# Performance work log

Measured on AMD Instinct MI355X. Metric: run time of the kernel, lower is better.

Reference implementation:

```python
import jax, jax.numpy as jnp
import numpy as np

D_MODEL = 1024
N_HEADS = 16
HEAD_DIM = D_MODEL // N_HEADS
B, T = 4, 2048


def setup_inputs() -> dict:
    key = jax.random.key(0)
    ks = jax.random.split(key, 5)
    s = 1.0 / np.sqrt(D_MODEL)
    return {
        "x": jax.random.normal(ks[0], (B, T, D_MODEL), dtype=jnp.float32),
        "Wq": jax.random.normal(ks[1], (D_MODEL, D_MODEL), dtype=jnp.float32) * s,
        "bq": jnp.zeros((D_MODEL,), jnp.float32),
        "Wk": jax.random.normal(ks[2], (D_MODEL, D_MODEL), dtype=jnp.float32) * s,
        "bk": jnp.zeros((D_MODEL,), jnp.float32),
        "Wv": jax.random.normal(ks[3], (D_MODEL, D_MODEL), dtype=jnp.float32) * s,
        "bv": jnp.zeros((D_MODEL,), jnp.float32),
        "Wo": jax.random.normal(ks[4], (D_MODEL, D_MODEL), dtype=jnp.float32) * s,
        "bo": jnp.zeros((D_MODEL,), jnp.float32),
    }


def reference(x, Wq, bq, Wk, bk, Wv, bv, Wo, bo):
    Bx, Tx, C = x.shape
    H, Dh = N_HEADS, HEAD_DIM
    # projections (torch Linear: y = x @ W.T + b)
    q = (x @ Wq.T + bq).reshape(Bx, Tx, H, Dh).transpose(0, 2, 1, 3)  # [B,H,T,Dh]
    k = (x @ Wk.T + bk).reshape(Bx, Tx, H, Dh).transpose(0, 2, 1, 3)
    v = (x @ Wv.T + bv).reshape(Bx, Tx, H, Dh).transpose(0, 2, 1, 3)
    scores = jnp.einsum("bhqd,bhkd->bhqk", q, k) / np.sqrt(Dh).astype(np.float32)
    causal = jnp.tril(jnp.ones((Tx, Tx), dtype=bool))
    scores = jnp.where(causal, scores, -jnp.inf)
    attn = jax.nn.softmax(scores, axis=-1)  # dropout in eval mode = identity
    y = jnp.einsum("bhqk,bhkd->bhqd", attn, v)
    y = y.transpose(0, 2, 1, 3).reshape(Bx, Tx, C)
    return y @ Wo.T + bo
```

## Files before the change

kernel.cpp:

```cpp
#include <hip/hip_runtime.h>

typedef __attribute__((ext_vector_type(8))) short short8;
typedef __attribute__((ext_vector_type(4))) float f32x4;
typedef unsigned short u16;
typedef unsigned int u32;

#define NH 16

#if __has_builtin(__builtin_amdgcn_exp2f)
#define EXP2(x) __builtin_amdgcn_exp2f(x)
#else
#define EXP2(x) exp2f(x)
#endif

__device__ __forceinline__ u32 f2bf(float f) {
  u32 u = __builtin_bit_cast(u32, f);
  return (u + 0x7fffu + ((u >> 16) & 1u)) >> 16;
}

__device__ __forceinline__ u32 cvtpk(float lo, float hi) {
  u32 r;
  asm("v_cvt_pk_bf16_f32 %0, %1, %2" : "=v"(r) : "v"(lo), "v"(hi));
  return r;
}

__device__ __forceinline__ void gload_lds16(const u16* g, u16* l) {
  __builtin_amdgcn_global_load_lds(
      (const __attribute__((address_space(1))) void*)g,
      (__attribute__((address_space(3))) void*)l, 16, 0, 0);
}

__global__ __launch_bounds__(256) void k_convert(
    const float* __restrict__ x, const float* __restrict__ wq,
    const float* __restrict__ wk, const float* __restrict__ wv,
    const float* __restrict__ wo, u16* __restrict__ dst) {
  int i = blockIdx.x * 256 + threadIdx.x;
  size_t e = (size_t)i * 4;
  const float* s; size_t off;
  if (e < 8388608ull)       { s = x;  off = e; }
  else if (e < 9437184ull)  { s = wq; off = e - 8388608ull; }
  else if (e < 10485760ull) { s = wk; off = e - 9437184ull; }
  else if (e < 11534336ull) { s = wv; off = e - 10485760ull; }
  else                      { s = wo; off = e - 11534336ull; }
  float4 d = *(const float4*)(s + off);
  uint2 o;
  o.x = cvtpk(d.x, d.y);
  o.y = cvtpk(d.z, d.w);
  *(uint2*)(dst + e) = o;
}

#define GPHASE(MH, NH_, LA, LB)                                                \
  if (LA) {                                                                    \
    _Pragma("unroll")                                                          \
    for (int mt = 0; mt < 4; ++mt)                                             \
      _Pragma("unroll")                                                        \
      for (int ks = 0; ks < 2; ++ks)                                           \
        af[mt][ks] = *(const short8*)(Ab +                                     \
            (wr * MT * 16 + ((MH) * 4 + mt) * 16 + l16) * 64 +                 \
            ((ks * 4 + quad) ^ swz) * 8);                                      \
  }                                                                            \
  if (LB) {                                                                    \
    _Pragma("unroll")                                                          \
    for (int nt = 0; nt < NH2; ++nt)                                           \
      _Pragma("unroll")                                                        \
      for (int ks = 0; ks < 2; ++ks)                                           \
        bfr[nt][ks] = *(const short8*)(Bb +                                    \
            (wn * NT * 16 + ((NH_) * NH2 + nt) * 16 + l16) * 64 +              \
            ((ks * 4 + quad) ^ swz) * 8);                                      \
  }                                                                            \
  __builtin_amdgcn_s_barrier();                                                \
  __builtin_amdgcn_s_setprio(1);                                               \
  _Pragma("unroll")                                                            \
  for (int mt = 0; mt < 4; ++mt)                                               \
    _Pragma("unroll")                                                          \
    for (int nt = 0; nt < NH2; ++nt)                                           \
      _Pragma("unroll")                                                        \
      for (int ks = 0; ks < 2; ++ks)                                           \
        acc[(MH) * 4 + mt][(NH_) * NH2 + nt] =                                 \
            __builtin_amdgcn_mfma_f32_16x16x32_bf16(                           \
                af[mt][ks], bfr[nt][ks], acc[(MH) * 4 + mt][(NH_) * NH2 + nt], \
                0, 0, 0);                                                      \
  __builtin_amdgcn_s_setprio(0);                                               \
  __builtin_amdgcn_s_barrier();                                                \
  __builtin_amdgcn_sched_barrier(0);

#define STAGE_T(T, PB)                                                         \
  {                                                                            \
    const u16* aT = aTh + (T) * 64;                                            \
    const u16* bT = bTh + (T) * 64;                                            \
    u16* aD = &As[PB][0] + dbase;                                              \
    u16* bD = &Bs[PB][0] + dbase;                                              \
    _Pragma("unroll")                                                          \
    for (int j = 0; j < NLA; ++j) gload_lds16(aT + j * 65536, aD + j * 4096);  \
    _Pragma("unroll")                                                          \
    for (int j = 0; j < NLB; ++j) gload_lds16(bT + j * 65536, bD + j * 4096);  \
  }

template <int MT, int NT>
__device__ __forceinline__ void gemm_core(const u16* __restrict__ Aptr,
                                          const u16* __restrict__ Bptr,
                                          int m0, int n0,
                                          f32x4 (&acc)[MT][NT]) {
  constexpr int NLA = MT / 2;
  constexpr int NLB = NT;
  constexpr int NLD = NLA + NLB;
  constexpr int NH2 = NT / 2;
  __shared__ u16 As[2][MT * 32 * 64];
  __shared__ u16 Bs[2][NT * 64 * 64];
  const int tid = threadIdx.x;
  const int wave = tid >> 6, lane = tid & 63;
  const int quad = lane >> 4, l16 = lane & 15;
  const int wr = wave >> 2, wn = wave & 3;
  const int swz = l16 & 7;
  const int srow = tid >> 3;
  const int srcg = (tid & 7) ^ (srow & 7);
  const u16* aTh = Aptr + (size_t)(m0 + srow) * 1024 + srcg * 8;
  const u16* bTh = Bptr + (size_t)(n0 + srow) * 1024 + srcg * 8;
  const int dbase = wave * 512;

  {
    f32x4 z = {0.f, 0.f, 0.f, 0.f};
    #pragma unroll
    for (int a = 0; a < MT; ++a)
      #pragma unroll
      for (int b2 = 0; b2 < NT; ++b2) acc[a][b2] = z;
  }

  STAGE_T(0, 0)

  short8 af[4][2], bfr[NH2][2];
  for (int t = 0; t < 16; ++t) {
    const int p = t & 1;
    if (t < 15) {
      STAGE_T(t + 1, p ^ 1)
      if constexpr (NLD == 8)
        asm volatile("s_waitcnt vmcnt(8)" ::: "memory");
      else if constexpr (NLD == 6)
        asm volatile("s_waitcnt vmcnt(6)" ::: "memory");
      else if constexpr (NLD == 4)
        asm volatile("s_waitcnt vmcnt(4)" ::: "memory");
      else
        asm volatile("s_waitcnt vmcnt(0)" ::: "memory");
    } else {
      asm volatile("s_waitcnt vmcnt(0)" ::: "memory");
    }
    __builtin_amdgcn_s_barrier();
    __builtin_amdgcn_sched_barrier(0);
    const u16* Ab = &As[p][0];
    const u16* Bb = &Bs[p][0];
    if constexpr (MT == 8) {
      GPHASE(0, 0, true, true)
      GPHASE(0, 1, false, true)
      GPHASE(1, 1, true, false)
      GPHASE(1, 0, false, true)
    } else {
      GPHASE(0, 0, true, true)
      GPHASE(0, 1, false, true)
    }
  }
}

__global__ __launch_bounds__(512, 2) void k_gemm_qkv(
    const u16* __restrict__ A, const u16* __restrict__ W,
    const float* __restrict__ bq, const float* __restrict__ bk,
    const float* __restrict__ bv, u16* __restrict__ qkv,
    u16* __restrict__ vt) {
  const int bid = blockIdx.x;
  const int xw = (bid & 7) * 96 + (bid >> 3);
  const int mtile = xw / 12, ntile = xw % 12;
  const int m0 = mtile * 128, n0 = ntile * 256;
  const int z = n0 >> 10;
  const float* bias = (z == 0) ? bq : (z == 1) ? bk : bv;
  u16* out = qkv + (size_t)z * 8388608;
  const float scl = (z == 0) ? 0.125f * 1.44269504088896340736f : 1.0f;
  f32x4 acc[4][4];
  gemm_core<4, 4>(A, W, m0, n0, acc);
  const int tid = threadIdx.x;
  const int wave = tid >> 6, lane = tid & 63;
  const int quad = lane >> 4, l16 = lane & 15;
  const int wr = wave >> 2, wn = wave & 3;
  if (z == 2) {
    #pragma unroll
    for (int mt = 0; mt < 4; ++mt) {
      #pragma unroll
      for (int nt = 0; nt < 4; ++nt) {
        int nn = (n0 + wn * 64 + nt * 16 + l16) & 1023;
        float bn = bias[nn];
        int h = nn >> 6, d = nn & 63;
        int mbase = m0 + wr * 64 + mt * 16 + quad * 4;
        int b = mbase >> 11, tb = mbase & 2047;
        uint2 pk;
        pk.x = cvtpk(acc[mt][nt][0] + bn, acc[mt][nt][1] + bn);
        pk.y = cvtpk(acc[mt][nt][2] + bn, acc[mt][nt][3] + bn);
        *(uint2*)(vt + ((size_t)(b * NH + h) * 64 + d) * 2048 + tb) = pk;
      }
    }
  } else {
    #pragma unroll
    for (int mt = 0; mt < 4; ++mt) {
      #pragma unroll
      for (int nt = 0; nt < 4; ++nt) {
        int nn = (n0 + wn * 64 + nt * 16 + l16) & 1023;
        float bn = bias[nn];
        int h = nn >> 6, d = nn & 63;
        #pragma unroll
        for (int r = 0; r < 4; ++r) {
          int m = m0 + wr * 64 + mt * 16 + quad * 4 + r;
          int b = m >> 11, tt = m & 2047;
          float val = (acc[mt][nt][r] + bn) * scl;
          out[(((size_t)(b * NH + h) * 2048 + tt) << 6) + d] = (u16)f2bf(val);
        }
      }
    }
  }
}

__global__ __launch_bounds__(512, 2) void k_gemm_out(
    const u16* __restrict__ A, const u16* __restrict__ Bw,
    const float* __restrict__ bias, float* __restrict__ out) {
  const int bid = blockIdx.x;
  const int sw = (bid & 7) * 32 + (bid >> 3);
  const int mtile = sw >> 3, ntile = sw & 7;
  const int m0 = mtile * 256, n0 = ntile * 128;
  f32x4 acc[8][2];
  gemm_core<8, 2>(A, Bw, m0, n0, acc);
  const int tid = threadIdx.x;
  const int wave = tid >> 6, lane = tid & 63;
  const int quad = lane >> 4, l16 = lane & 15;
  const int wr = wave >> 2, wn = wave & 3;
  #pragma unroll
  for (int mt = 0; mt < 8; ++mt) {
    #pragma unroll
    for (int nt = 0; nt < 2; ++nt) {
      int n = n0 + wn * 32 + nt * 16 + l16;
      float bn = bias[n];
      #pragma unroll
      for (int r = 0; r < 4; ++r) {
        int m = m0 + wr * 128 + mt * 16 + quad * 4 + r;
        out[(size_t)m * 1024 + n] = acc[mt][nt][r] + bn;
      }
    }
  }
}

#define ATTN_SUB(P, QF0, QF1, O, MI, LI, DIAG)                                 \
  {                                                                            \
    f32x4 st[4];                                                               \
    _Pragma("unroll")                                                          \
    for (int nt = 0; nt < 4; ++nt) {                                           \
      short8 kf0 = *(const short8*)(&Ks[P][(nt * 16 + l16) * 72 + quad * 8]);  \
      short8 kf1 = *(const short8*)(&Ks[P][(nt * 16 + l16) * 72 + 32 + quad * 8]); \
      f32x4 z4 = {0.f, 0.f, 0.f, 0.f};                                         \
      z4 = __builtin_amdgcn_mfma_f32_16x16x32_bf16(kf0, QF0, z4, 0, 0, 0);     \
      st[nt] = __builtin_amdgcn_mfma_f32_16x16x32_bf16(kf1, QF1, z4, 0, 0, 0); \
    }                                                                          \
    if (DIAG) {                                                                \
      int q_loc = wave * 16 + l16;                                             \
      _Pragma("unroll")                                                        \
      for (int nt = 0; nt < 4; ++nt) {                                         \
        _Pragma("unroll")                                                      \
        for (int r = 0; r < 4; ++r) {                                          \
          int k_loc = nt * 16 + quad * 4 + r;                                  \
          if (k_loc > q_loc) st[nt][r] = -1e30f;                               \
        }                                                                      \
      }                                                                        \
    }                                                                          \
    float mq[4];                                                               \
    _Pragma("unroll")                                                          \
    for (int nt = 0; nt < 4; ++nt)                                             \
      mq[nt] = fmaxf(fmaxf(st[nt][0], st[nt][1]), fmaxf(st[nt][2], st[nt][3]));\
    float mx = fmaxf(fmaxf(mq[0], mq[1]), fmaxf(mq[2], mq[3]));                \
    mx = fmaxf(mx, __shfl_xor(mx, 16, 64));                                    \
    mx = fmaxf(mx, __shfl_xor(mx, 32, 64));                                    \
    float mnew = fmaxf(MI, mx);                                                \
    float alpha = EXP2(MI - mnew);                                             \
    MI = mnew;                                                                 \
    LI *= alpha;                                                               \
    _Pragma("unroll")                                                          \
    for (int r = 0; r < 4; ++r) {                                              \
      float av = __shfl(alpha, quad * 4 + r, 16);                              \
      _Pragma("unroll")                                                        \
      for (int dt = 0; dt < 4; ++dt) O[dt][r] *= av;                           \
    }                                                                          \
    u32 Wx[4], Wy[4];                                                          \
    float sq[4];                                                               \
    _Pragma("unroll")                                                          \
    for (int nt = 0; nt < 4; ++nt) {                                           \
      float p0 = EXP2(st[nt][0] - mnew);                                       \
      float p1 = EXP2(st[nt][1] - mnew);                                       \
      float p2 = EXP2(st[nt][2] - mnew);                                       \
      float p3 = EXP2(st[nt][3] - mnew);                                       \
      sq[nt] = (p0 + p1) + (p2 + p3);                                          \
      Wx[nt] = cvtpk(p0, p1);                                                  \
      Wy[nt] = cvtpk(p2, p3);                                                  \
    }                                                                          \
    float sum = (sq[0] + sq[1]) + (sq[2] + sq[3]);                             \
    sum += __shfl_xor(sum, 16, 64);                                            \
    sum += __shfl_xor(sum, 32, 64);                                            \
    LI += sum;                                                                 \
    uint4 t0, t1;                                                              \
    {                                                                          \
      u32 e, f;                                                                \
      e = __shfl(Wx[0], s0, 64); f = __shfl(Wx[1], s0, 64); t0.x = hi ? f : e; \
      e = __shfl(Wy[0], s0, 64); f = __shfl(Wy[1], s0, 64); t0.y = hi ? f : e; \
      e = __shfl(Wx[0], s1, 64); f = __shfl(Wx[1], s1, 64); t0.z = hi ? f : e; \
      e = __shfl(Wy[0], s1, 64); f = __shfl(Wy[1], s1, 64); t0.w = hi ? f : e; \
      e = __shfl(Wx[2], s0, 64); f = __shfl(Wx[3], s0, 64); t1.x = hi ? f : e; \
      e = __shfl(Wy[2], s0, 64); f = __shfl(Wy[3], s0, 64); t1.y = hi ? f : e; \
      e = __shfl(Wx[2], s1, 64); f = __shfl(Wx[3], s1, 64); t1.z = hi ? f : e; \
      e = __shfl(Wy[2], s1, 64); f = __shfl(Wy[3], s1, 64); t1.w = hi ? f : e; \
    }                                                                          \
    short8 pf0 = __builtin_bit_cast(short8, t0);                               \
    short8 pf1 = __builtin_bit_cast(short8, t1);                               \
    _Pragma("unroll")                                                          \
    for (int dt = 0; dt < 4; ++dt) {                                           \
      short8 vf0 = *(const short8*)(&Vs[P][(dt * 16 + l16) * 72 + quad * 8]);  \
      short8 vf1 = *(const short8*)(&Vs[P][(dt * 16 + l16) * 72 + 32 + quad * 8]); \
      O[dt] = __builtin_amdgcn_mfma_f32_16x16x32_bf16(pf0, vf0, O[dt], 0, 0, 0); \
      O[dt] = __builtin_amdgcn_mfma_f32_16x16x32_bf16(pf1, vf1, O[dt], 0, 0, 0); \
    }                                                                          \
  }

#define ATTN_EPI(O, LI, QT)                                                    \
  _Pragma("unroll")                                                            \
  for (int r = 0; r < 4; ++r) {                                                \
    float lv = __shfl(LI, quad * 4 + r, 16);                                   \
    float inv = 1.0f / lv;                                                     \
    int t = (QT) * 64 + wave * 16 + quad * 4 + r;                              \
    _Pragma("unroll")                                                          \
    for (int dt = 0; dt < 4; ++dt) {                                           \
      int d = dt * 16 + l16;                                                   \
      y[(((size_t)b * 2048 + t) * NH + h) * 64 + d] = (u16)f2bf(O[dt][r] * inv); \
    }                                                                          \
  }

__global__ __launch_bounds__(256, 4) void k_attn(
    const u16* __restrict__ q, const u16* __restrict__ k,
    const u16* __restrict__ vt, u16* __restrict__ y) {
  const int tid = threadIdx.x;
  const int wave = tid >> 6, lane = tid & 63;
  const int quad = lane >> 4, l16 = lane & 15;
  const int bh = blockIdx.x, bx = blockIdx.y;
  const int qtB = bx, qtA = 31 - bx;
  const int b = bh >> 4, h = bh & 15;

  __shared__ u16 Ks[2][64 * 72];
  __shared__ u16 Vs[2][64 * 72];

  const u16* qbA = q + ((size_t)bh * 2048 + qtA * 64 + wave * 16 + l16) * 64;
  short8 qA0 = *(const short8*)(qbA + quad * 8);
  short8 qA1 = *(const short8*)(qbA + 32 + quad * 8);
  const u16* qbB = q + ((size_t)bh * 2048 + qtB * 64 + wave * 16 + l16) * 64;
  short8 qB0 = *(const short8*)(qbB + quad * 8);
  short8 qB1 = *(const short8*)(qbB + 32 + quad * 8);

  f32x4 oA[4], oB[4];
  {
    f32x4 z = {0.f, 0.f, 0.f, 0.f};
    #pragma unroll
    for (int dt = 0; dt < 4; ++dt) { oA[dt] = z; oB[dt] = z; }
  }
  float mA = -1e30f, lA = 0.f, mB = -1e30f, lB = 0.f;

  const u16* kbase = k + (size_t)bh * 131072;
  const u16* vbase = vt + (size_t)bh * 131072;
  const int r0 = tid >> 3, cc = tid & 7;
  const int s0 = ((quad & 1) << 5) + l16, s1 = s0 + 16;
  const int hi = quad >> 1;

  {
    uint4 k0 = *(const uint4*)(kbase + (size_t)r0 * 64 + cc * 8);
    uint4 k1 = *(const uint4*)(kbase + (size_t)(r0 + 32) * 64 + cc * 8);
    uint4 v0 = *(const uint4*)(vbase + (size_t)r0 * 2048 + cc * 8);
    uint4 v1 = *(const uint4*)(vbase + (size_t)(r0 + 32) * 2048 + cc * 8);
    *(uint4*)(&Ks[0][r0 * 72 + cc * 8]) = k0;
    *(uint4*)(&Ks[0][(r0 + 32) * 72 + cc * 8]) = k1;
    *(uint4*)(&Vs[0][r0 * 72 + cc * 8]) = v0;
    *(uint4*)(&Vs[0][(r0 + 32) * 72 + cc * 8]) = v1;
  }
  __syncthreads();

  for (int kt = 0; kt <= qtA; ++kt) {
    const int p = kt & 1;
    const bool pre = (kt < qtA);
    uint4 kr0, kr1, vr0, vr1;
    if (pre) {
      const u16* kb = kbase + (size_t)(kt + 1) * 4096;
      const u16* vb = vbase + (kt + 1) * 64;
      kr0 = *(const uint4*)(kb + (size_t)r0 * 64 + cc * 8);
      kr1 = *(const uint4*)(kb + (size_t)(r0 + 32) * 64 + cc * 8);
      vr0 = *(const uint4*)(vb + (size_t)r0 * 2048 + cc * 8);
      vr1 = *(const uint4*)(vb + (size_t)(r0 + 32) * 2048 + cc * 8);
    }

    ATTN_SUB(p, qA0, qA1, oA, mA, lA, (kt == qtA))
    if (kt <= qtB) {
      ATTN_SUB(p, qB0, qB1, oB, mB, lB, (kt == qtB))
    }

    if (pre) {
      *(uint4*)(&Ks[p ^ 1][r0 * 72 + cc * 8]) = kr0;
      *(uint4*)(&Ks[p ^ 1][(r0 + 32) * 72 + cc * 8]) = kr1;
      *(uint4*)(&Vs[p ^ 1][r0 * 72 + cc * 8]) = vr0;
      *(uint4*)(&Vs[p ^ 1][(r0 + 32) * 72 + cc * 8]) = vr1;
    }
    __syncthreads();
  }

  ATTN_EPI(oA, lA, qtA)
  ATTN_EPI(oB, lB, qtB)
}

extern "C" void kernel_launch(void* const* d_in, const int* in_sizes, int n_in,
                              void* d_out, int out_size, void* d_ws, size_t ws_size,
                              hipStream_t stream) {
  const float* x  = (const float*)d_in[0];
  const float* Wq = (const float*)d_in[1];
  const float* bq = (const float*)d_in[2];
  const float* Wk = (const float*)d_in[3];
  const float* bk = (const float*)d_in[4];
  const float* Wv = (const float*)d_in[5];
  const float* bv = (const float*)d_in[6];
  const float* Wo = (const float*)d_in[7];
  const float* bo = (const float*)d_in[8];
  float* out = (float*)d_out;

  u16* ws  = (u16*)d_ws;
  u16* xb  = ws;
  u16* Wb  = ws + 8388608;
  u16* qkv = ws + 12582912;
  u16* vt  = ws + 37748736;
  u16* y   = ws + 46137344;

  k_convert<<<dim3(12288), dim3(256), 0, stream>>>(x, Wq, Wk, Wv, Wo, ws);
  k_gemm_qkv<<<dim3(768), dim3(512), 0, stream>>>(xb, Wb, bq, bk, bv, qkv, vt);
  k_attn<<<dim3(64, 16), dim3(256), 0, stream>>>(qkv, qkv + 8388608, vt, y);
  k_gemm_out<<<dim3(256), dim3(512), 0, stream>>>(y, Wb + 3 * 1048576, bo, out);
}
```

Baseline: 297.5 us.

## Load K/V fragments directly from global memory and retile output GEMM

The attention kernel drops the LDS double-buffered K/V staging and its per-iteration barriers. Each wave now loads its MFMA K and V fragments straight from global memory into registers, relying on L1/L2 reuse across the four waves. The loop is also split into QK, softmax and PV stages so the two query tiles can interleave. Separately, the output projection GEMM changes its tile from 256x128 to 128x256. This trades LDS traffic and sync for more global/cache load instructions and higher register pressure.

```diff
diff --git a/kernel.cpp b/kernel.cpp
--- a/kernel.cpp
+++ b/kernel.cpp
@@ -220,39 +220,36 @@
     const float* __restrict__ bias, float* __restrict__ out) {
   const int bid = blockIdx.x;
   const int sw = (bid & 7) * 32 + (bid >> 3);
-  const int mtile = sw >> 3, ntile = sw & 7;
-  const int m0 = mtile * 256, n0 = ntile * 128;
-  f32x4 acc[8][2];
-  gemm_core<8, 2>(A, Bw, m0, n0, acc);
+  const int mtile = sw >> 2, ntile = sw & 3;
+  const int m0 = mtile * 128, n0 = ntile * 256;
+  f32x4 acc[4][4];
+  gemm_core<4, 4>(A, Bw, m0, n0, acc);
   const int tid = threadIdx.x;
   const int wave = tid >> 6, lane = tid & 63;
   const int quad = lane >> 4, l16 = lane & 15;
   const int wr = wave >> 2, wn = wave & 3;
   #pragma unroll
-  for (int mt = 0; mt < 8; ++mt) {
-    #pragma unroll
-    for (int nt = 0; nt < 2; ++nt) {
-      int n = n0 + wn * 32 + nt * 16 + l16;
+  for (int mt = 0; mt < 4; ++mt) {
+    #pragma unroll
+    for (int nt = 0; nt < 4; ++nt) {
+      int n = n0 + wn * 64 + nt * 16 + l16;
       float bn = bias[n];
       #pragma unroll
       for (int r = 0; r < 4; ++r) {
-        int m = m0 + wr * 128 + mt * 16 + quad * 4 + r;
+        int m = m0 + wr * 64 + mt * 16 + quad * 4 + r;
         out[(size_t)m * 1024 + n] = acc[mt][nt][r] + bn;
       }
     }
   }
 }
 
-#define ATTN_SUB(P, QF0, QF1, O, MI, LI, DIAG)                                 \
+#define QK_STEP(KF, QF0, QF1, ST, DIAG)                                        \
   {                                                                            \
-    f32x4 st[4];                                                               \
     _Pragma("unroll")                                                          \
     for (int nt = 0; nt < 4; ++nt) {                                           \
-      short8 kf0 = *(const short8*)(&Ks[P][(nt * 16 + l16) * 72 + quad * 8]);  \
-      short8 kf1 = *(const short8*)(&Ks[P][(nt * 16 + l16) * 72 + 32 + quad * 8]); \
       f32x4 z4 = {0.f, 0.f, 0.f, 0.f};                                         \
-      z4 = __builtin_amdgcn_mfma_f32_16x16x32_bf16(kf0, QF0, z4, 0, 0, 0);     \
-      st[nt] = __builtin_amdgcn_mfma_f32_16x16x32_bf16(kf1, QF1, z4, 0, 0, 0); \
+      z4 = __builtin_amdgcn_mfma_f32_16x16x32_bf16(KF[nt][0], QF0, z4, 0, 0, 0); \
+      ST[nt] = __builtin_amdgcn_mfma_f32_16x16x32_bf16(KF[nt][1], QF1, z4, 0, 0, 0); \
     }                                                                          \
     if (DIAG) {                                                                \
       int q_loc = wave * 16 + l16;                                             \
@@ -261,14 +258,18 @@
         _Pragma("unroll")                                                      \
         for (int r = 0; r < 4; ++r) {                                          \
           int k_loc = nt * 16 + quad * 4 + r;                                  \
-          if (k_loc > q_loc) st[nt][r] = -1e30f;                               \
+          if (k_loc > q_loc) ST[nt][r] = -1e30f;                               \
         }                                                                      \
       }                                                                        \
     }                                                                          \
+  }
+
+#define SM_STEP(ST, MI, LI, O, PF0, PF1)                                       \
+  {                                                                            \
     float mq[4];                                                               \
     _Pragma("unroll")                                                          \
     for (int nt = 0; nt < 4; ++nt)                                             \
-      mq[nt] = fmaxf(fmaxf(st[nt][0], st[nt][1]), fmaxf(st[nt][2], st[nt][3]));\
+      mq[nt] = fmaxf(fmaxf(ST[nt][0], ST[nt][1]), fmaxf(ST[nt][2], ST[nt][3]));\
     float mx = fmaxf(fmaxf(mq[0], mq[1]), fmaxf(mq[2], mq[3]));                \
     mx = fmaxf(mx, __shfl_xor(mx, 16, 64));                                    \
     mx = fmaxf(mx, __shfl_xor(mx, 32, 64));                                    \
@@ -286,10 +287,10 @@
     float sq[4];                                                               \
     _Pragma("unroll")                                                          \
     for (int nt = 0; nt < 4; ++nt) {                                           \
-      float p0 = EXP2(st[nt][0] - mnew);                                       \
-      float p1 = EXP2(st[nt][1] - mnew);                                       \
-      float p2 = EXP2(st[nt][2] - mnew);                                       \
-      float p3 = EXP2(st[nt][3] - mnew);                                       \
+      float p0 = EXP2(ST[nt][0] - mnew);                                       \
+      float p1 = EXP2(ST[nt][1] - mnew);                                       \
+      float p2 = EXP2(ST[nt][2] - mnew);                                       \
+      float p3 = EXP2(ST[nt][3] - mnew);                                       \
       sq[nt] = (p0 + p1) + (p2 + p3);                                          \
       Wx[nt] = cvtpk(p0, p1);                                                  \
       Wy[nt] = cvtpk(p2, p3);                                                  \
@@ -310,14 +311,16 @@
       e = __shfl(Wx[2], s1, 64); f = __shfl(Wx[3], s1, 64); t1.z = hi ? f : e; \
       e = __shfl(Wy[2], s1, 64); f = __shfl(Wy[3], s1, 64); t1.w = hi ? f : e; \
     }                                                                          \
-    short8 pf0 = __builtin_bit_cast(short8, t0);                               \
-    short8 pf1 = __builtin_bit_cast(short8, t1);                               \
+    PF0 = __builtin_bit_cast(short8, t0);                                      \
+    PF1 = __builtin_bit_cast(short8, t1);                                      \
+  }
+
+#define PV_STEP(VF, PF0, PF1, O)                                               \
+  {                                                                            \
     _Pragma("unroll")                                                          \
     for (int dt = 0; dt < 4; ++dt) {                                           \
-      short8 vf0 = *(const short8*)(&Vs[P][(dt * 16 + l16) * 72 + quad * 8]);  \
-      short8 vf1 = *(const short8*)(&Vs[P][(dt * 16 + l16) * 72 + 32 + quad * 8]); \
-      O[dt] = __builtin_amdgcn_mfma_f32_16x16x32_bf16(pf0, vf0, O[dt], 0, 0, 0); \
-      O[dt] = __builtin_amdgcn_mfma_f32_16x16x32_bf16(pf1, vf1, O[dt], 0, 0, 0); \
+      O[dt] = __builtin_amdgcn_mfma_f32_16x16x32_bf16(PF0, VF[dt][0], O[dt], 0, 0, 0); \
+      O[dt] = __builtin_amdgcn_mfma_f32_16x16x32_bf16(PF1, VF[dt][1], O[dt], 0, 0, 0); \
     }                                                                          \
   }
 
@@ -344,9 +347,6 @@
   const int qtB = bx, qtA = 31 - bx;
   const int b = bh >> 4, h = bh & 15;
 
-  __shared__ u16 Ks[2][64 * 72];
-  __shared__ u16 Vs[2][64 * 72];
-
   const u16* qbA = q + ((size_t)bh * 2048 + qtA * 64 + wave * 16 + l16) * 64;
   short8 qA0 = *(const short8*)(qbA + quad * 8);
   short8 qA1 = *(const short8*)(qbA + 32 + quad * 8);
@@ -362,49 +362,33 @@
   }
   float mA = -1e30f, lA = 0.f, mB = -1e30f, lB = 0.f;
 
-  const u16* kbase = k + (size_t)bh * 131072;
-  const u16* vbase = vt + (size_t)bh * 131072;
-  const int r0 = tid >> 3, cc = tid & 7;
+  const u16* kp = k + (size_t)bh * 131072 + (size_t)l16 * 64 + quad * 8;
+  const u16* vp = vt + (size_t)bh * 131072 + (size_t)l16 * 2048 + quad * 8;
   const int s0 = ((quad & 1) << 5) + l16, s1 = s0 + 16;
   const int hi = quad >> 1;
 
-  {
-    uint4 k0 = *(const uint4*)(kbase + (size_t)r0 * 64 + cc * 8);
-    uint4 k1 = *(const uint4*)(kbase + (size_t)(r0 + 32) * 64 + cc * 8);
-    uint4 v0 = *(const uint4*)(vbase + (size_t)r0 * 2048 + cc * 8);
-    uint4 v1 = *(const uint4*)(vbase + (size_t)(r0 + 32) * 2048 + cc * 8);
-    *(uint4*)(&Ks[0][r0 * 72 + cc * 8]) = k0;
-    *(uint4*)(&Ks[0][(r0 + 32) * 72 + cc * 8]) = k1;
-    *(uint4*)(&Vs[0][r0 * 72 + cc * 8]) = v0;
-    *(uint4*)(&Vs[0][(r0 + 32) * 72 + cc * 8]) = v1;
-  }
-  __syncthreads();
-
-  for (int kt = 0; kt <= qtA; ++kt) {
-    const int p = kt & 1;
-    const bool pre = (kt < qtA);
-    uint4 kr0, kr1, vr0, vr1;
-    if (pre) {
-      const u16* kb = kbase + (size_t)(kt + 1) * 4096;
-      const u16* vb = vbase + (kt + 1) * 64;
-      kr0 = *(const uint4*)(kb + (size_t)r0 * 64 + cc * 8);
-      kr1 = *(const uint4*)(kb + (size_t)(r0 + 32) * 64 + cc * 8);
-      vr0 = *(const uint4*)(vb + (size_t)r0 * 2048 + cc * 8);
-      vr1 = *(const uint4*)(vb + (size_t)(r0 + 32) * 2048 + cc * 8);
-    }
-
-    ATTN_SUB(p, qA0, qA1, oA, mA, lA, (kt == qtA))
-    if (kt <= qtB) {
-      ATTN_SUB(p, qB0, qB1, oB, mB, lB, (kt == qtB))
-    }
-
-    if (pre) {
-      *(uint4*)(&Ks[p ^ 1][r0 * 72 + cc * 8]) = kr0;
-      *(uint4*)(&Ks[p ^ 1][(r0 + 32) * 72 + cc * 8]) = kr1;
-      *(uint4*)(&Vs[p ^ 1][r0 * 72 + cc * 8]) = vr0;
-      *(uint4*)(&Vs[p ^ 1][(r0 + 32) * 72 + cc * 8]) = vr1;
-    }
-    __syncthreads();
+  for (int kt = 0; kt <= qtA; ++kt, kp += 4096, vp += 64) {
+    const bool doB = (kt <= qtB);
+    short8 kf[4][2];
+    #pragma unroll
+    for (int nt = 0; nt < 4; ++nt) {
+      kf[nt][0] = *(const short8*)(kp + nt * 1024);
+      kf[nt][1] = *(const short8*)(kp + nt * 1024 + 32);
+    }
+    f32x4 stA[4], stB[4];
+    QK_STEP(kf, qA0, qA1, stA, (kt == qtA))
+    if (doB) { QK_STEP(kf, qB0, qB1, stB, (kt == qtB)) }
+    short8 vf[4][2];
+    #pragma unroll
+    for (int dt = 0; dt < 4; ++dt) {
+      vf[dt][0] = *(const short8*)(vp + (size_t)dt * 32768);
+      vf[dt][1] = *(const short8*)(vp + (size_t)dt * 32768 + 32);
+    }
+    short8 pfA0, pfA1, pfB0, pfB1;
+    SM_STEP(stA, mA, lA, oA, pfA0, pfA1)
+    if (doB) { SM_STEP(stB, mB, lB, oB, pfB0, pfB1) }
+    PV_STEP(vf, pfA0, pfA1, oA)
+    if (doB) { PV_STEP(vf, pfB0, pfB1, oB) }
   }
 
   ATTN_EPI(oA, lA, qtA)
```

Result: slower. 426.6 us (+43.4%).

## Specialize GEMM core to 128x256 tiles and split staging loads across phases

Applied to the files above, without the earlier changes.

Replaces the templated GEMM core with a single 128x256 variant used by both the QKV and output projections. The output projection moves from 256x128 to 128x256 tiles with a new tile mapping. Next-tile global-to-LDS loads are split into two halves, one issued before and one between the two MFMA phases, with a lighter vmcnt wait. The aim is to spread memory traffic across the compute phases and unify the tile shape. The risk is that the second half-load may not complete before the next iteration's wait, and that the output GEMM's tile count and shape change its occupancy.

```diff
diff --git a/kernel.cpp b/kernel.cpp
--- a/kernel.cpp
+++ b/kernel.cpp
@@ -49,64 +49,59 @@
   *(uint2*)(dst + e) = o;
 }
 
-#define GPHASE(MH, NH_, LA, LB)                                                \
+#define GP44(NH_, LA)                                                          \
   if (LA) {                                                                    \
     _Pragma("unroll")                                                          \
     for (int mt = 0; mt < 4; ++mt)                                             \
       _Pragma("unroll")                                                        \
       for (int ks = 0; ks < 2; ++ks)                                           \
-        af[mt][ks] = *(const short8*)(Ab +                                     \
-            (wr * MT * 16 + ((MH) * 4 + mt) * 16 + l16) * 64 +                 \
-            ((ks * 4 + quad) ^ swz) * 8);                                      \
+        af[mt][ks] = *(const short8*)(Ab + (wr * 64 + mt * 16 + l16) * 64 +    \
+                                      ((ks * 4 + quad) ^ swz) * 8);            \
   }                                                                            \
-  if (LB) {                                                                    \
-    _Pragma("unroll")                                                          \
-    for (int nt = 0; nt < NH2; ++nt)                                           \
-      _Pragma("unroll")                                                        \
-      for (int ks = 0; ks < 2; ++ks)                                           \
-        bfr[nt][ks] = *(const short8*)(Bb +                                    \
-            (wn * NT * 16 + ((NH_) * NH2 + nt) * 16 + l16) * 64 +              \
-            ((ks * 4 + quad) ^ swz) * 8);                                      \
-  }                                                                            \
+  _Pragma("unroll")                                                            \
+  for (int nt = 0; nt < 2; ++nt)                                               \
+    _Pragma("unroll")                                                          \
+    for (int ks = 0; ks < 2; ++ks)                                             \
+      bfr[nt][ks] = *(const short8*)(                                          \
+          Bb + (wn * 64 + ((NH_) * 2 + nt) * 16 + l16) * 64 +                  \
+          ((ks * 4 + quad) ^ swz) * 8);                                        \
   __builtin_amdgcn_s_barrier();                                                \
   __builtin_amdgcn_s_setprio(1);                                               \
   _Pragma("unroll")                                                            \
   for (int mt = 0; mt < 4; ++mt)                                               \
     _Pragma("unroll")                                                          \
-    for (int nt = 0; nt < NH2; ++nt)                                           \
+    for (int nt = 0; nt < 2; ++nt)                                             \
       _Pragma("unroll")                                                        \
       for (int ks = 0; ks < 2; ++ks)                                           \
-        acc[(MH) * 4 + mt][(NH_) * NH2 + nt] =                                 \
-            __builtin_amdgcn_mfma_f32_16x16x32_bf16(                           \
-                af[mt][ks], bfr[nt][ks], acc[(MH) * 4 + mt][(NH_) * NH2 + nt], \
-                0, 0, 0);                                                      \
+        acc[mt][(NH_) * 2 + nt] = __builtin_amdgcn_mfma_f32_16x16x32_bf16(     \
+            af[mt][ks], bfr[nt][ks], acc[mt][(NH_) * 2 + nt], 0, 0, 0);        \
   __builtin_amdgcn_s_setprio(0);                                               \
   __builtin_amdgcn_s_barrier();                                                \
   __builtin_amdgcn_sched_barrier(0);
 
-#define STAGE_T(T, PB)                                                         \
+#define SH0(T, PB)                                                             \
   {                                                                            \
     const u16* aT = aTh + (T) * 64;                                            \
     const u16* bT = bTh + (T) * 64;                                            \
-    u16* aD = &As[PB][0] + dbase;                                              \
-    u16* bD = &Bs[PB][0] + dbase;                                              \
-    _Pragma("unroll")                                                          \
-    for (int j = 0; j < NLA; ++j) gload_lds16(aT + j * 65536, aD + j * 4096);  \
-    _Pragma("unroll")                                                          \
-    for (int j = 0; j < NLB; ++j) gload_lds16(bT + j * 65536, bD + j * 4096);  \
-  }
-
-template <int MT, int NT>
-__device__ __forceinline__ void gemm_core(const u16* __restrict__ Aptr,
-                                          const u16* __restrict__ Bptr,
-                                          int m0, int n0,
-                                          f32x4 (&acc)[MT][NT]) {
-  constexpr int NLA = MT / 2;
-  constexpr int NLB = NT;
-  constexpr int NLD = NLA + NLB;
-  constexpr int NH2 = NT / 2;
-  __shared__ u16 As[2][MT * 32 * 64];
-  __shared__ u16 Bs[2][NT * 64 * 64];
+    gload_lds16(aT, &As[PB][dbase]);                                           \
+    gload_lds16(bT, &Bs[PB][dbase]);                                           \
+    gload_lds16(bT + 65536, &Bs[PB][dbase + 4096]);                            \
+  }
+#define SH1(T, PB)                                                             \
+  {                                                                            \
+    const u16* aT = aTh + (T) * 64;                                            \
+    const u16* bT = bTh + (T) * 64;                                            \
+    gload_lds16(aT + 65536, &As[PB][dbase + 4096]);                            \
+    gload_lds16(bT + 131072, &Bs[PB][dbase + 8192]);                           \
+    gload_lds16(bT + 196608, &Bs[PB][dbase + 12288]);                          \
+  }
+
+__device__ __forceinline__ void gemm_core44(const u16* __restrict__ Aptr,
+                                            const u16* __restrict__ Bptr,
+                                            int m0, int n0,
+                                            f32x4 (&acc)[4][4]) {
+  __shared__ u16 As[2][8192];
+  __shared__ u16 Bs[2][16384];
   const int tid = threadIdx.x;
   const int wave = tid >> 6, lane = tid & 63;
   const int quad = lane >> 4, l16 = lane & 15;
@@ -121,26 +116,20 @@
   {
     f32x4 z = {0.f, 0.f, 0.f, 0.f};
     #pragma unroll
-    for (int a = 0; a < MT; ++a)
+    for (int a = 0; a < 4; ++a)
       #pragma unroll
-      for (int b2 = 0; b2 < NT; ++b2) acc[a][b2] = z;
-  }
-
-  STAGE_T(0, 0)
-
-  short8 af[4][2], bfr[NH2][2];
+      for (int b2 = 0; b2 < 4; ++b2) acc[a][b2] = z;
+  }
+
+  SH0(0, 0)
+  SH1(0, 0)
+
+  short8 af[4][2], bfr[2][2];
   for (int t = 0; t < 16; ++t) {
     const int p = t & 1;
     if (t < 15) {
-      STAGE_T(t + 1, p ^ 1)
-      if constexpr (NLD == 8)
-        asm volatile("s_waitcnt vmcnt(8)" ::: "memory");
-      else if constexpr (NLD == 6)
-        asm volatile("s_waitcnt vmcnt(6)" ::: "memory");
-      else if constexpr (NLD == 4)
-        asm volatile("s_waitcnt vmcnt(4)" ::: "memory");
-      else
-        asm volatile("s_waitcnt vmcnt(0)" ::: "memory");
+      SH0(t + 1, p ^ 1)
+      asm volatile("s_waitcnt vmcnt(3)" ::: "memory");
     } else {
       asm volatile("s_waitcnt vmcnt(0)" ::: "memory");
     }
@@ -148,15 +137,9 @@
     __builtin_amdgcn_sched_barrier(0);
     const u16* Ab = &As[p][0];
     const u16* Bb = &Bs[p][0];
-    if constexpr (MT == 8) {
-      GPHASE(0, 0, true, true)
-      GPHASE(0, 1, false, true)
-      GPHASE(1, 1, true, false)
-      GPHASE(1, 0, false, true)
-    } else {
-      GPHASE(0, 0, true, true)
-      GPHASE(0, 1, false, true)
-    }
+    GP44(0, true)
+    if (t < 15) SH1(t + 1, p ^ 1)
+    GP44(1, false)
   }
 }
 
@@ -174,7 +157,7 @@
   u16* out = qkv + (size_t)z * 8388608;
   const float scl = (z == 0) ? 0.125f * 1.44269504088896340736f : 1.0f;
   f32x4 acc[4][4];
-  gemm_core<4, 4>(A, W, m0, n0, acc);
+  gemm_core44(A, W, m0, n0, acc);
   const int tid = threadIdx.x;
   const int wave = tid >> 6, lane = tid & 63;
   const int quad = lane >> 4, l16 = lane & 15;
@@ -220,23 +203,23 @@
     const float* __restrict__ bias, float* __restrict__ out) {
   const int bid = blockIdx.x;
   const int sw = (bid & 7) * 32 + (bid >> 3);
-  const int mtile = sw >> 3, ntile = sw & 7;
-  const int m0 = mtile * 256, n0 = ntile * 128;
-  f32x4 acc[8][2];
-  gemm_core<8, 2>(A, Bw, m0, n0, acc);
+  const int mtile = sw >> 2, ntile = sw & 3;
+  const int m0 = mtile * 128, n0 = ntile * 256;
+  f32x4 acc[4][4];
+  gemm_core44(A, Bw, m0, n0, acc);
   const int tid = threadIdx.x;
   const int wave = tid >> 6, lane = tid & 63;
   const int quad = lane >> 4, l16 = lane & 15;
   const int wr = wave >> 2, wn = wave & 3;
   #pragma unroll
-  for (int mt = 0; mt < 8; ++mt) {
+  for (int mt = 0; mt < 4; ++mt) {
     #pragma unroll
-    for (int nt = 0; nt < 2; ++nt) {
-      int n = n0 + wn * 32 + nt * 16 + l16;
+    for (int nt = 0; nt < 4; ++nt) {
+      int n = n0 + wn * 64 + nt * 16 + l16;
       float bn = bias[n];
       #pragma unroll
       for (int r = 0; r < 4; ++r) {
-        int m = m0 + wr * 128 + mt * 16 + quad * 4 + r;
+        int m = m0 + wr * 64 + mt * 16 + quad * 4 + r;
         out[(size_t)m * 1024 + n] = acc[mt][nt][r] + bn;
       }
     }
```

Result: slower. 313.0 us (+5.2%).
